# Kernel optimization log

Hardware: AMD Instinct MI355X
Metric: run time of the kernel (lower is better)

The kernel has to match this reference:

```python
import jax, jax.numpy as jnp
import numpy as np

B, T, D_MODEL, D_HIDDEN, MAX_SEQLEN = 4, 2048, 1024, 1024, 2048


def setup_inputs() -> dict:
    key = jax.random.key(0)
    ks = jax.random.split(key, 8)
    scale = 0.02  # keep exp() and linear outputs in a sane range
    return {
        "q": jax.random.normal(ks[0], (B, T, D_MODEL), dtype=jnp.float32),
        "k": jax.random.normal(ks[1], (B, T, D_MODEL), dtype=jnp.float32),
        "v": jax.random.normal(ks[2], (B, T, D_MODEL), dtype=jnp.float32),
        "Wq": jax.random.normal(ks[3], (D_HIDDEN, D_MODEL), dtype=jnp.float32) * scale,
        "Wk": jax.random.normal(ks[4], (D_HIDDEN, D_MODEL), dtype=jnp.float32) * scale,
        "Wv": jax.random.normal(ks[5], (D_HIDDEN, D_MODEL), dtype=jnp.float32) * scale,
        "Wo": jax.random.normal(ks[6], (D_MODEL, D_HIDDEN), dtype=jnp.float32) * scale,
        "W_bias": jax.random.normal(ks[7], (MAX_SEQLEN, MAX_SEQLEN), dtype=jnp.float32) * scale,
    }


def reference(q, k, v, Wq, Wk, Wv, Wo, W_bias):
    Ti = q.shape[1]
    Tj = k.shape[1]
    # Linear projections (torch Linear: x @ W.T), bias=False
    Q = jnp.einsum('btm,hm->bth', q, Wq)
    K = jnp.einsum('btm,hm->bth', k, Wk)
    V = jnp.einsum('btm,hm->bth', v, Wv)
    pos_bias = W_bias[:Ti, :Tj][None]              # (1, Ti, Tj)
    # Faithful to original: max over dim 0 (batch dim for K, singleton dim for pos_bias)
    max_key = jnp.max(K, axis=0, keepdims=True)    # (1, Tj, Dh)
    max_pos_bias = jnp.max(pos_bias, axis=0, keepdims=True)  # == pos_bias (dim 0 is size 1)
    exp_key = jnp.exp(K - max_key)                 # (B, Tj, Dh)
    exp_pos_bias = jnp.exp(pos_bias - max_pos_bias)  # all-ones, kept for faithfulness
    num = jnp.einsum('bij,bjd->bid', exp_pos_bias, exp_key * V)
    den = jnp.einsum('bij,bjd->bid', exp_pos_bias, exp_key)
    Yt = jax.nn.sigmoid(Q) * num / den             # (B, Ti, Dh)
    return jnp.einsum('bth,mh->btm', Yt, Wo)
```

## Files before the change

### kernel.cpp

```cpp
#include <hip/hip_runtime.h>
#include <hip/hip_bf16.h>

typedef __bf16 bf16;
typedef __bf16 bf16x8 __attribute__((ext_vector_type(8)));
typedef float f32x4 __attribute__((ext_vector_type(4)));
typedef float f32x16 __attribute__((ext_vector_type(16)));

#define B_   4
#define T_   2048
#define DM_  1024
#define DH_  1024
#define MROWS 8192

struct CvtJob { const float* src; bf16* dst; int nf4; };
struct CvtArgs { CvtJob job[7]; };

__global__ __launch_bounds__(256) void cvt_kernel(CvtArgs args) {
  CvtJob jb = args.job[blockIdx.y];
  int base = blockIdx.x * 2048;
  if (base >= jb.nf4) return;
  int t2 = threadIdx.x * 2;
  const float4* s = (const float4*)jb.src;
  float4 a[4][2];
#pragma unroll
  for (int u = 0; u < 4; ++u) {
    a[u][0] = s[base + u * 512 + t2];
    a[u][1] = s[base + u * 512 + t2 + 1];
  }
#pragma unroll
  for (int u = 0; u < 4; ++u) {
    bf16x8 o;
    o[0] = (bf16)a[u][0].x; o[1] = (bf16)a[u][0].y;
    o[2] = (bf16)a[u][0].z; o[3] = (bf16)a[u][0].w;
    o[4] = (bf16)a[u][1].x; o[5] = (bf16)a[u][1].y;
    o[6] = (bf16)a[u][1].z; o[7] = (bf16)a[u][1].w;
    *(bf16x8*)(jb.dst + ((size_t)base + u * 512 + t2) * 4) = o;
  }
}

struct GemmJob { const bf16* A; const bf16* Bw; float* Cf; bf16* Cb; int mode; };
struct GemmArgs { GemmJob job[4]; int N; int K; };

template <int MT>
__global__ __launch_bounds__(256) void gemm_bt(GemmArgs ga) {
  const GemmJob jb = ga.job[blockIdx.z];
  const int N = ga.N, K = ga.K;
  constexpr int TM = MT * 64;
  __shared__ __align__(16) bf16 As[TM * 64];
  __shared__ __align__(16) bf16 Bs[128 * 64];

  const int tid  = threadIdx.x;
  const int lane = tid & 63;
  const int wave = tid >> 6;
  const int wm   = (wave >> 1) * (MT * 32);
  const int wn   = (wave & 1) * 64;

  const int f   = blockIdx.y * 8 + blockIdx.x;
  const int xcd = f & 7;
  const int j   = f >> 3;
  const int bn  = j & 7;
  const int bm  = (j >> 3) * 8 + xcd;
  const int tileM = bm * TM;
  const int tileN = bn * 128;

  f32x16 acc[MT][2] = {};

  const int sr = lane >> 3;

  const char* pa = (const char*)(jb.A  + (size_t)tileM * K);
  const char* pb = (const char*)(jb.Bw + (size_t)tileN * K);
  unsigned int offA[MT * 2], offB[4];
#pragma unroll
  for (int l = 0; l < MT * 2; ++l) {
    int grp = wave * (MT * 2) + l;
    int sc  = (lane & 7) ^ sr ^ (grp & 7);
    offA[l] = (unsigned int)(((grp * 8 + sr) * K + sc * 8) * 2);
  }
#pragma unroll
  for (int l = 0; l < 4; ++l) {
    int grp = wave * 4 + l;
    int sc  = (lane & 7) ^ sr ^ (grp & 7);
    offB[l] = (unsigned int)(((grp * 8 + sr) * K + sc * 8) * 2);
  }

  const int half = lane >> 5;
  const int rc   = lane & 31;

  for (int k0 = 0; k0 < K; k0 += 64) {
#pragma unroll
    for (int l = 0; l < MT * 2; ++l)
      __builtin_amdgcn_global_load_lds(
          (const __attribute__((address_space(1))) void*)(pa + offA[l]),
          (__attribute__((address_space(3))) void*)&As[(wave * (MT * 2) + l) * 512],
          16, 0, 0);
#pragma unroll
    for (int l = 0; l < 4; ++l)
      __builtin_amdgcn_global_load_lds(
          (const __attribute__((address_space(1))) void*)(pb + offB[l]),
          (__attribute__((address_space(3))) void*)&Bs[(wave * 4 + l) * 512],
          16, 0, 0);
    pa += 128;
    pb += 128;
    __syncthreads();

#pragma unroll
    for (int s = 0; s < 2; ++s) {
      bf16x8 af[MT][2], bfr[2][2];
#pragma unroll
      for (int mt = 0; mt < MT; ++mt)
#pragma unroll
        for (int kk = 0; kk < 2; ++kk) {
          int row = wm + mt * 32 + rc;
          int chunk = ((s * 2 + kk) * 2 + half) ^ (row & 7) ^ ((row >> 3) & 7);
          af[mt][kk] = *(const bf16x8*)&As[row * 64 + chunk * 8];
        }
#pragma unroll
      for (int nt = 0; nt < 2; ++nt)
#pragma unroll
        for (int kk = 0; kk < 2; ++kk) {
          int row = wn + nt * 32 + rc;
          int chunk = ((s * 2 + kk) * 2 + half) ^ (row & 7) ^ ((row >> 3) & 7);
          bfr[nt][kk] = *(const bf16x8*)&Bs[row * 64 + chunk * 8];
        }
#pragma unroll
      for (int kk = 0; kk < 2; ++kk)
#pragma unroll
        for (int mt = 0; mt < MT; ++mt)
#pragma unroll
          for (int nt = 0; nt < 2; ++nt)
            acc[mt][nt] = __builtin_amdgcn_mfma_f32_32x32x16_bf16(
                af[mt][kk], bfr[nt][kk], acc[mt][nt], 0, 0, 0);
    }
    __syncthreads();
  }

  const int cn    = rc;
  const int rbase = half * 4;
  if (jb.mode == 0) {
#pragma unroll
    for (int mt = 0; mt < MT; ++mt)
#pragma unroll
      for (int nt = 0; nt < 2; ++nt)
#pragma unroll
        for (int r = 0; r < 16; ++r) {
          int row = tileM + wm + mt * 32 + rbase + (r & 3) + 8 * (r >> 2);
          int col = tileN + wn + nt * 32 + cn;
          jb.Cf[(size_t)row * N + col] = acc[mt][nt][r];
        }
  } else if (jb.mode == 1) {
#pragma unroll
    for (int mt = 0; mt < MT; ++mt)
#pragma unroll
      for (int nt = 0; nt < 2; ++nt)
#pragma unroll
        for (int r = 0; r < 16; ++r) {
          int row = tileM + wm + mt * 32 + rbase + (r & 3) + 8 * (r >> 2);
          int col = tileN + wn + nt * 32 + cn;
          jb.Cb[(size_t)row * N + col] =
              (bf16)(1.f / (1.f + __expf(-acc[mt][nt][r])));
        }
  } else {
#pragma unroll
    for (int mt = 0; mt < MT; ++mt)
#pragma unroll
      for (int nt = 0; nt < 2; ++nt)
#pragma unroll
        for (int r = 0; r < 16; ++r) {
          int row = tileM + wm + mt * 32 + rbase + (r & 3) + 8 * (r >> 2);
          int col = tileN + wn + nt * 32 + cn;
          jb.Cb[(size_t)row * N + col] = (bf16)acc[mt][nt][r];
        }
  }
}

__global__ __launch_bounds__(256) void kv_fused(
    const bf16* __restrict__ Ak, const bf16* __restrict__ Wk,
    const bf16* __restrict__ Av, const bf16* __restrict__ Wv,
    float* __restrict__ part) {
  const int K = DM_;
  __shared__ __align__(16) bf16 As[128 * 64];
  __shared__ __align__(16) bf16 Bs[128 * 64];

  const int tid  = threadIdx.x;
  const int lane = tid & 63;
  const int wave = tid >> 6;
  const int wm   = (wave >> 1) * 64;
  const int wn   = (wave & 1) * 64;

  const int f   = blockIdx.y * 8 + blockIdx.x;
  const int xcd = f & 7;
  const int j   = f >> 3;
  const int bn  = j & 7;
  const int bm  = (j >> 3) * 8 + xcd;
  const int tileN = bn * 128;
  const int j0    = bm * 32;

  const int sr   = lane >> 3;
  const int half = lane >> 5;
  const int rc   = lane & 31;

  unsigned int offA[4], offB[4];
#pragma unroll
  for (int l = 0; l < 4; ++l) {
    int grp = wave * 4 + l;
    int tr  = grp * 8 + sr;
    int sc  = (lane & 7) ^ sr ^ (grp & 7);
    offA[l] = (unsigned int)((((tr >> 5) * T_ + j0 + (tr & 31)) * K + sc * 8) * 2);
    offB[l] = (unsigned int)(((grp * 8 + sr) * K + sc * 8) * 2);
  }

  auto run = [&](const char* pa, const char* pb, f32x16 (&acc)[2][2]) {
    for (int k0 = 0; k0 < K; k0 += 64) {
#pragma unroll
      for (int l = 0; l < 4; ++l)
        __builtin_amdgcn_global_load_lds(
            (const __attribute__((address_space(1))) void*)(pa + offA[l]),
            (__attribute__((address_space(3))) void*)&As[(wave * 4 + l) * 512],
            16, 0, 0);
#pragma unroll
      for (int l = 0; l < 4; ++l)
        __builtin_amdgcn_global_load_lds(
            (const __attribute__((address_space(1))) void*)(pb + offB[l]),
            (__attribute__((address_space(3))) void*)&Bs[(wave * 4 + l) * 512],
            16, 0, 0);
      pa += 128;
      pb += 128;
      __syncthreads();
#pragma unroll
      for (int s = 0; s < 2; ++s) {
        bf16x8 af[2][2], bfr[2][2];
#pragma unroll
        for (int mt = 0; mt < 2; ++mt)
#pragma unroll
          for (int kk = 0; kk < 2; ++kk) {
            int row = wm + mt * 32 + rc;
            int chunk = ((s * 2 + kk) * 2 + half) ^ (row & 7) ^ ((row >> 3) & 7);
            af[mt][kk] = *(const bf16x8*)&As[row * 64 + chunk * 8];
          }
#pragma unroll
        for (int nt = 0; nt < 2; ++nt)
#pragma unroll
          for (int kk = 0; kk < 2; ++kk) {
            int row = wn + nt * 32 + rc;
            int chunk = ((s * 2 + kk) * 2 + half) ^ (row & 7) ^ ((row >> 3) & 7);
            bfr[nt][kk] = *(const bf16x8*)&Bs[row * 64 + chunk * 8];
          }
#pragma unroll
        for (int kk = 0; kk < 2; ++kk)
#pragma unroll
          for (int mt = 0; mt < 2; ++mt)
#pragma unroll
            for (int nt = 0; nt < 2; ++nt)
              acc[mt][nt] = __builtin_amdgcn_mfma_f32_32x32x16_bf16(
                  af[mt][kk], bfr[nt][kk], acc[mt][nt], 0, 0, 0);
      }
      __syncthreads();
    }
  };

  f32x16 aK[2][2] = {}, aV[2][2] = {};
  run((const char*)Ak, (const char*)(Wk + (size_t)tileN * K), aK);
  run((const char*)Av, (const char*)(Wv + (size_t)tileN * K), aV);

  const int rbase = half * 4;
  float* mx01 = (float*)As;
  float* mx23 = (float*)Bs;
#pragma unroll
  for (int nt = 0; nt < 2; ++nt)
#pragma unroll
    for (int r = 0; r < 16; ++r) {
      float ml = fmaxf(aK[0][nt][r], aK[1][nt][r]);
      int jloc = rbase + (r & 3) + 8 * (r >> 2);
      int idx  = (wave & 1) * 2048 + jloc * 64 + nt * 32 + rc;
      if (wave < 2) mx01[idx] = ml; else mx23[idx] = ml;
    }
  __syncthreads();
  float sn[2][2] = {{0.f, 0.f}, {0.f, 0.f}};
  float sd[2][2] = {{0.f, 0.f}, {0.f, 0.f}};
#pragma unroll
  for (int nt = 0; nt < 2; ++nt)
#pragma unroll
    for (int r = 0; r < 16; ++r) {
      int jloc = rbase + (r & 3) + 8 * (r >> 2);
      int idx  = (wave & 1) * 2048 + jloc * 64 + nt * 32 + rc;
      float mo = (wave < 2) ? mx23[idx] : mx01[idx];
      float m  = fmaxf(fmaxf(aK[0][nt][r], aK[1][nt][r]), mo);
      float e0 = __expf(aK[0][nt][r] - m);
      float e1 = __expf(aK[1][nt][r] - m);
      sn[0][nt] += e0 * aV[0][nt][r];
      sn[1][nt] += e1 * aV[1][nt][r];
      sd[0][nt] += e0;
      sd[1][nt] += e1;
    }
#pragma unroll
  for (int mt = 0; mt < 2; ++mt)
#pragma unroll
    for (int nt = 0; nt < 2; ++nt) {
      float n = sn[mt][nt] + __shfl_xor(sn[mt][nt], 32, 64);
      float d = sd[mt][nt] + __shfl_xor(sd[mt][nt], 32, 64);
      int b    = (wave >> 1) * 2 + mt;
      int dcol = tileN + wn + nt * 32 + rc;
      size_t base = (size_t)bm * 8192 + (size_t)b * 1024 + dcol;
      if (lane < 32) part[base] = n;
      else           part[base + 4096] = d;
    }
}

__global__ __launch_bounds__(256) void finish_kv(
    const float* __restrict__ part, float* __restrict__ numden) {
  int slot = blockIdx.x * 256 + threadIdx.x;
  float s0 = 0.f, s1 = 0.f, s2 = 0.f, s3 = 0.f;
#pragma unroll
  for (int i = 0; i < 64; i += 4) {
    s0 += part[(size_t)(i + 0) * 8192 + slot];
    s1 += part[(size_t)(i + 1) * 8192 + slot];
    s2 += part[(size_t)(i + 2) * 8192 + slot];
    s3 += part[(size_t)(i + 3) * 8192 + slot];
  }
  numden[slot] = (s0 + s1) + (s2 + s3);
}

__global__ __launch_bounds__(256) void scale_wo(
    const bf16* __restrict__ Wo, const float* __restrict__ numden,
    bf16* __restrict__ out4) {
  const int b = blockIdx.y;
  size_t i = ((size_t)blockIdx.x * 256 + threadIdx.x) * 8;
  int h = (int)(i & (DH_ - 1));
  bf16x8 w = *(const bf16x8*)(Wo + i);
  const float* nu = numden + b * DH_ + h;
  const float* de = numden + 4096 + b * DH_ + h;
  float4 n0 = *(const float4*)nu;
  float4 n1 = *(const float4*)(nu + 4);
  float4 d0 = *(const float4*)de;
  float4 d1 = *(const float4*)(de + 4);
  bf16x8 o;
  o[0] = (bf16)((float)w[0] * n0.x / d0.x);
  o[1] = (bf16)((float)w[1] * n0.y / d0.y);
  o[2] = (bf16)((float)w[2] * n0.z / d0.z);
  o[3] = (bf16)((float)w[3] * n0.w / d0.w);
  o[4] = (bf16)((float)w[4] * n1.x / d1.x);
  o[5] = (bf16)((float)w[5] * n1.y / d1.y);
  o[6] = (bf16)((float)w[6] * n1.z / d1.z);
  o[7] = (bf16)((float)w[7] * n1.w / d1.w);
  *(bf16x8*)(out4 + (size_t)b * ((size_t)DM_ * DH_) + i) = o;
}

extern "C" void kernel_launch(void* const* d_in, const int* in_sizes, int n_in,
                              void* d_out, int out_size, void* d_ws, size_t ws_size,
                              hipStream_t stream) {
  const float* q  = (const float*)d_in[0];
  const float* k  = (const float*)d_in[1];
  const float* v  = (const float*)d_in[2];
  const float* Wq = (const float*)d_in[3];
  const float* Wk = (const float*)d_in[4];
  const float* Wv = (const float*)d_in[5];
  const float* Wo = (const float*)d_in[6];
  float* out = (float*)d_out;

  char* ws = (char*)d_ws;
  size_t off = 0;
  auto alloc = [&](size_t bytes) {
    char* p = ws + off;
    off += (bytes + 255) & ~(size_t)255;
    return p;
  };
  const size_t actN = (size_t)MROWS * DM_;
  const size_t wN   = (size_t)DH_ * DM_;

  bf16* qb  = (bf16*)alloc(actN * 2);
  bf16* kb  = (bf16*)alloc(actN * 2);
  bf16* vb  = (bf16*)alloc(actN * 2);
  bf16* Wqb = (bf16*)alloc(wN * 2);
  bf16* Wkb = (bf16*)alloc(wN * 2);
  bf16* Wvb = (bf16*)alloc(wN * 2);
  bf16* Wob = (bf16*)alloc(wN * 2);
  bf16* Yb  = (bf16*)alloc(actN * 2);
  float* part = (float*)alloc((size_t)64 * 8192 * 4);
  float* numden = (float*)alloc(8192 * 4);
  bf16* Wob4 = (bf16*)alloc((size_t)B_ * wN * 2);

  CvtArgs ca;
  ca.job[0] = {q,  qb,  (int)(actN / 4)};
  ca.job[1] = {k,  kb,  (int)(actN / 4)};
  ca.job[2] = {v,  vb,  (int)(actN / 4)};
  ca.job[3] = {Wq, Wqb, (int)(wN / 4)};
  ca.job[4] = {Wk, Wkb, (int)(wN / 4)};
  ca.job[5] = {Wv, Wvb, (int)(wN / 4)};
  ca.job[6] = {Wo, Wob, (int)(wN / 4)};
  cvt_kernel<<<dim3(actN / 4 / 2048, 7), 256, 0, stream>>>(ca);

  GemmArgs g1;
  g1.N = DH_; g1.K = DM_;
  g1.job[0] = {qb, Wqb, nullptr, Yb, 1};
  g1.job[1] = {nullptr, nullptr, nullptr, nullptr, 0};
  g1.job[2] = {nullptr, nullptr, nullptr, nullptr, 0};
  g1.job[3] = {nullptr, nullptr, nullptr, nullptr, 0};
  gemm_bt<2><<<dim3(8, 64, 1), 256, 0, stream>>>(g1);

  kv_fused<<<dim3(8, 64), 256, 0, stream>>>(kb, Wkb, vb, Wvb, part);

  finish_kv<<<dim3(32), 256, 0, stream>>>(part, numden);

  scale_wo<<<dim3(512, 4), 256, 0, stream>>>(Wob, numden, Wob4);

  GemmArgs g2;
  g2.N = DM_; g2.K = DH_;
  for (int b = 0; b < 4; ++b) {
    g2.job[b] = {Yb + (size_t)b * ((size_t)T_ * DH_),
                 Wob4 + (size_t)b * wN,
                 out + (size_t)b * ((size_t)T_ * DM_),
                 nullptr, 0};
  }
  gemm_bt<1><<<dim3(8, 32, 4), 256, 0, stream>>>(g2);
}
```

Baseline: 286.7 us.

## Merge Q projection and KV reduction into one launch with smaller KV tiles

Replaces the separate Q-projection GEMM and the KV fused kernel with a single kernel whose grid splits into Q-GEMM blocks and KV blocks. KV blocks now cover 16 sequence positions across all 4 batches per tile, so the batch max is computed in registers without an LDS exchange. This raises the KV block count from 512 to 1024 to fill the GPU better and removes one launch, letting Q and KV work run concurrently. In exchange the KV blocks use half-height A tiles (less reuse of the weight tile), and there are four times as many partial slabs, so finish_kv does a longer reduction.

```diff
diff --git a/kernel.cpp b/kernel.cpp
--- a/kernel.cpp
+++ b/kernel.cpp
@@ -38,6 +38,213 @@
   }
 }
 
+__global__ __launch_bounds__(256) void proj_fused(
+    const bf16* __restrict__ qA, const bf16* __restrict__ qW,
+    bf16* __restrict__ Yb,
+    const bf16* __restrict__ kA, const bf16* __restrict__ kW,
+    const bf16* __restrict__ vA, const bf16* __restrict__ vW,
+    float* __restrict__ part) {
+  const int K = DM_;
+  __shared__ __align__(16) bf16 As[128 * 64];
+  __shared__ __align__(16) bf16 Bs[128 * 64];
+
+  const int tid  = threadIdx.x;
+  const int lane = tid & 63;
+  const int wave = tid >> 6;
+  const int sr   = lane >> 3;
+  const int half = lane >> 5;
+  const int rc   = lane & 31;
+  const int wn   = (wave & 1) * 64;
+
+  if (blockIdx.y < 64) {
+    const int wm  = (wave >> 1) * 64;
+    const int f   = blockIdx.y * 8 + blockIdx.x;
+    const int xcd = f & 7;
+    const int j   = f >> 3;
+    const int bn  = j & 7;
+    const int bm  = (j >> 3) * 8 + xcd;
+    const int tileM = bm * 128;
+    const int tileN = bn * 128;
+
+    f32x16 acc[2][2] = {};
+    const char* pa = (const char*)(qA + (size_t)tileM * K);
+    const char* pb = (const char*)(qW + (size_t)tileN * K);
+    unsigned int off[4];
+#pragma unroll
+    for (int l = 0; l < 4; ++l) {
+      int grp = wave * 4 + l;
+      int sc  = (lane & 7) ^ sr ^ (grp & 7);
+      off[l] = (unsigned int)(((grp * 8 + sr) * K + sc * 8) * 2);
+    }
+
+    for (int k0 = 0; k0 < K; k0 += 64) {
+#pragma unroll
+      for (int l = 0; l < 4; ++l)
+        __builtin_amdgcn_global_load_lds(
+            (const __attribute__((address_space(1))) void*)(pa + off[l]),
+            (__attribute__((address_space(3))) void*)&As[(wave * 4 + l) * 512],
+            16, 0, 0);
+#pragma unroll
+      for (int l = 0; l < 4; ++l)
+        __builtin_amdgcn_global_load_lds(
+            (const __attribute__((address_space(1))) void*)(pb + off[l]),
+            (__attribute__((address_space(3))) void*)&Bs[(wave * 4 + l) * 512],
+            16, 0, 0);
+      pa += 128;
+      pb += 128;
+      __syncthreads();
+#pragma unroll
+      for (int s = 0; s < 2; ++s) {
+        bf16x8 af[2][2], bfr[2][2];
+#pragma unroll
+        for (int mt = 0; mt < 2; ++mt)
+#pragma unroll
+          for (int kk = 0; kk < 2; ++kk) {
+            int row = wm + mt * 32 + rc;
+            int chunk = ((s * 2 + kk) * 2 + half) ^ (row & 7) ^ ((row >> 3) & 7);
+            af[mt][kk] = *(const bf16x8*)&As[row * 64 + chunk * 8];
+          }
+#pragma unroll
+        for (int nt = 0; nt < 2; ++nt)
+#pragma unroll
+          for (int kk = 0; kk < 2; ++kk) {
+            int row = wn + nt * 32 + rc;
+            int chunk = ((s * 2 + kk) * 2 + half) ^ (row & 7) ^ ((row >> 3) & 7);
+            bfr[nt][kk] = *(const bf16x8*)&Bs[row * 64 + chunk * 8];
+          }
+#pragma unroll
+        for (int kk = 0; kk < 2; ++kk)
+#pragma unroll
+          for (int mt = 0; mt < 2; ++mt)
+#pragma unroll
+            for (int nt = 0; nt < 2; ++nt)
+              acc[mt][nt] = __builtin_amdgcn_mfma_f32_32x32x16_bf16(
+                  af[mt][kk], bfr[nt][kk], acc[mt][nt], 0, 0, 0);
+      }
+      __syncthreads();
+    }
+
+    const int rbase = half * 4;
+#pragma unroll
+    for (int mt = 0; mt < 2; ++mt)
+#pragma unroll
+      for (int nt = 0; nt < 2; ++nt)
+#pragma unroll
+        for (int r = 0; r < 16; ++r) {
+          int row = tileM + wm + mt * 32 + rbase + (r & 3) + 8 * (r >> 2);
+          int col = tileN + wn + nt * 32 + rc;
+          Yb[(size_t)row * DH_ + col] =
+              (bf16)(1.f / (1.f + __expf(-acc[mt][nt][r])));
+        }
+    return;
+  }
+
+  const int wm  = (wave >> 1) * 32;
+  const int g   = (blockIdx.y - 64) * 8 + blockIdx.x;
+  const int xcd = g & 7;
+  const int h   = g >> 3;
+  const int bn  = h & 7;
+  const int jt  = (h >> 3) * 8 + xcd;
+  const int tileN = bn * 128;
+  const int j0    = jt * 16;
+
+  unsigned int offA[2], offB[4];
+#pragma unroll
+  for (int l = 0; l < 2; ++l) {
+    int grp = wave * 2 + l;
+    int tr  = grp * 8 + sr;
+    int sc  = (lane & 7) ^ sr ^ (grp & 7);
+    int rg  = (tr & 3) * T_ + j0 + (tr >> 2);
+    offA[l] = (unsigned int)(((size_t)rg * K + sc * 8) * 2);
+  }
+#pragma unroll
+  for (int l = 0; l < 4; ++l) {
+    int grp = wave * 4 + l;
+    int sc  = (lane & 7) ^ sr ^ (grp & 7);
+    offB[l] = (unsigned int)(((grp * 8 + sr) * K + sc * 8) * 2);
+  }
+
+  auto run = [&](const char* pa, const char* pb, f32x16 (&acc)[2]) {
+    for (int k0 = 0; k0 < K; k0 += 64) {
+#pragma unroll
+      for (int l = 0; l < 2; ++l)
+        __builtin_amdgcn_global_load_lds(
+            (const __attribute__((address_space(1))) void*)(pa + offA[l]),
+            (__attribute__((address_space(3))) void*)&As[(wave * 2 + l) * 512],
+            16, 0, 0);
+#pragma unroll
+      for (int l = 0; l < 4; ++l)
+        __builtin_amdgcn_global_load_lds(
+            (const __attribute__((address_space(1))) void*)(pb + offB[l]),
+            (__attribute__((address_space(3))) void*)&Bs[(wave * 4 + l) * 512],
+            16, 0, 0);
+      pa += 128;
+      pb += 128;
+      __syncthreads();
+#pragma unroll
+      for (int s = 0; s < 2; ++s) {
+        bf16x8 af[2], bfr[2][2];
+#pragma unroll
+        for (int kk = 0; kk < 2; ++kk) {
+          int row = wm + rc;
+          int chunk = ((s * 2 + kk) * 2 + half) ^ (row & 7) ^ ((row >> 3) & 7);
+          af[kk] = *(const bf16x8*)&As[row * 64 + chunk * 8];
+        }
+#pragma unroll
+        for (int nt = 0; nt < 2; ++nt)
+#pragma unroll
+          for (int kk = 0; kk < 2; ++kk) {
+            int row = wn + nt * 32 + rc;
+            int chunk = ((s * 2 + kk) * 2 + half) ^ (row & 7) ^ ((row >> 3) & 7);
+            bfr[nt][kk] = *(const bf16x8*)&Bs[row * 64 + chunk * 8];
+          }
+#pragma unroll
+        for (int kk = 0; kk < 2; ++kk)
+#pragma unroll
+          for (int nt = 0; nt < 2; ++nt)
+            acc[nt] = __builtin_amdgcn_mfma_f32_32x32x16_bf16(
+                af[kk], bfr[nt][kk], acc[nt], 0, 0, 0);
+      }
+      __syncthreads();
+    }
+  };
+
+  f32x16 aK[2] = {}, aV[2] = {};
+  run((const char*)kA, (const char*)(kW + (size_t)tileN * K), aK);
+  run((const char*)vA, (const char*)(vW + (size_t)tileN * K), aV);
+
+  float num[4][2] = {}, den[4][2] = {};
+#pragma unroll
+  for (int nt = 0; nt < 2; ++nt)
+#pragma unroll
+    for (int s = 0; s < 4; ++s) {
+      float m = fmaxf(fmaxf(aK[nt][4 * s + 0], aK[nt][4 * s + 1]),
+                      fmaxf(aK[nt][4 * s + 2], aK[nt][4 * s + 3]));
+#pragma unroll
+      for (int b = 0; b < 4; ++b) {
+        float e = __expf(aK[nt][4 * s + b] - m);
+        num[b][nt] += e * aV[nt][4 * s + b];
+        den[b][nt] += e;
+      }
+    }
+#pragma unroll
+  for (int b = 0; b < 4; ++b)
+#pragma unroll
+    for (int nt = 0; nt < 2; ++nt) {
+      num[b][nt] += __shfl_xor(num[b][nt], 32, 64);
+      den[b][nt] += __shfl_xor(den[b][nt], 32, 64);
+    }
+  const int slab = jt * 2 + (wave >> 1);
+#pragma unroll
+  for (int b = 0; b < 4; ++b)
+#pragma unroll
+    for (int nt = 0; nt < 2; ++nt) {
+      size_t base = (size_t)slab * 8192 + b * 1024 + tileN + wn + nt * 32 + rc;
+      if (lane < 32) part[base] = num[b][nt];
+      else           part[base + 4096] = den[b][nt];
+    }
+}
+
 struct GemmJob { const bf16* A; const bf16* Bw; float* Cf; bf16* Cb; int mode; };
 struct GemmArgs { GemmJob job[4]; int N; int K; };
 
@@ -64,7 +271,6 @@
   const int tileN = bn * 128;
 
   f32x16 acc[MT][2] = {};
-
   const int sr = lane >> 3;
 
   const char* pa = (const char*)(jb.A  + (size_t)tileM * K);
@@ -173,145 +379,11 @@
   }
 }
 
-__global__ __launch_bounds__(256) void kv_fused(
-    const bf16* __restrict__ Ak, const bf16* __restrict__ Wk,
-    const bf16* __restrict__ Av, const bf16* __restrict__ Wv,
-    float* __restrict__ part) {
-  const int K = DM_;
-  __shared__ __align__(16) bf16 As[128 * 64];
-  __shared__ __align__(16) bf16 Bs[128 * 64];
-
-  const int tid  = threadIdx.x;
-  const int lane = tid & 63;
-  const int wave = tid >> 6;
-  const int wm   = (wave >> 1) * 64;
-  const int wn   = (wave & 1) * 64;
-
-  const int f   = blockIdx.y * 8 + blockIdx.x;
-  const int xcd = f & 7;
-  const int j   = f >> 3;
-  const int bn  = j & 7;
-  const int bm  = (j >> 3) * 8 + xcd;
-  const int tileN = bn * 128;
-  const int j0    = bm * 32;
-
-  const int sr   = lane >> 3;
-  const int half = lane >> 5;
-  const int rc   = lane & 31;
-
-  unsigned int offA[4], offB[4];
-#pragma unroll
-  for (int l = 0; l < 4; ++l) {
-    int grp = wave * 4 + l;
-    int tr  = grp * 8 + sr;
-    int sc  = (lane & 7) ^ sr ^ (grp & 7);
-    offA[l] = (unsigned int)((((tr >> 5) * T_ + j0 + (tr & 31)) * K + sc * 8) * 2);
-    offB[l] = (unsigned int)(((grp * 8 + sr) * K + sc * 8) * 2);
-  }
-
-  auto run = [&](const char* pa, const char* pb, f32x16 (&acc)[2][2]) {
-    for (int k0 = 0; k0 < K; k0 += 64) {
-#pragma unroll
-      for (int l = 0; l < 4; ++l)
-        __builtin_amdgcn_global_load_lds(
-            (const __attribute__((address_space(1))) void*)(pa + offA[l]),
-            (__attribute__((address_space(3))) void*)&As[(wave * 4 + l) * 512],
-            16, 0, 0);
-#pragma unroll
-      for (int l = 0; l < 4; ++l)
-        __builtin_amdgcn_global_load_lds(
-            (const __attribute__((address_space(1))) void*)(pb + offB[l]),
-            (__attribute__((address_space(3))) void*)&Bs[(wave * 4 + l) * 512],
-            16, 0, 0);
-      pa += 128;
-      pb += 128;
-      __syncthreads();
-#pragma unroll
-      for (int s = 0; s < 2; ++s) {
-        bf16x8 af[2][2], bfr[2][2];
-#pragma unroll
-        for (int mt = 0; mt < 2; ++mt)
-#pragma unroll
-          for (int kk = 0; kk < 2; ++kk) {
-            int row = wm + mt * 32 + rc;
-            int chunk = ((s * 2 + kk) * 2 + half) ^ (row & 7) ^ ((row >> 3) & 7);
-            af[mt][kk] = *(const bf16x8*)&As[row * 64 + chunk * 8];
-          }
-#pragma unroll
-        for (int nt = 0; nt < 2; ++nt)
-#pragma unroll
-          for (int kk = 0; kk < 2; ++kk) {
-            int row = wn + nt * 32 + rc;
-            int chunk = ((s * 2 + kk) * 2 + half) ^ (row & 7) ^ ((row >> 3) & 7);
-            bfr[nt][kk] = *(const bf16x8*)&Bs[row * 64 + chunk * 8];
-          }
-#pragma unroll
-        for (int kk = 0; kk < 2; ++kk)
-#pragma unroll
-          for (int mt = 0; mt < 2; ++mt)
-#pragma unroll
-            for (int nt = 0; nt < 2; ++nt)
-              acc[mt][nt] = __builtin_amdgcn_mfma_f32_32x32x16_bf16(
-                  af[mt][kk], bfr[nt][kk], acc[mt][nt], 0, 0, 0);
-      }
-      __syncthreads();
-    }
-  };
-
-  f32x16 aK[2][2] = {}, aV[2][2] = {};
-  run((const char*)Ak, (const char*)(Wk + (size_t)tileN * K), aK);
-  run((const char*)Av, (const char*)(Wv + (size_t)tileN * K), aV);
-
-  const int rbase = half * 4;
-  float* mx01 = (float*)As;
-  float* mx23 = (float*)Bs;
-#pragma unroll
-  for (int nt = 0; nt < 2; ++nt)
-#pragma unroll
-    for (int r = 0; r < 16; ++r) {
-      float ml = fmaxf(aK[0][nt][r], aK[1][nt][r]);
-      int jloc = rbase + (r & 3) + 8 * (r >> 2);
-      int idx  = (wave & 1) * 2048 + jloc * 64 + nt * 32 + rc;
-      if (wave < 2) mx01[idx] = ml; else mx23[idx] = ml;
-    }
-  __syncthreads();
-  float sn[2][2] = {{0.f, 0.f}, {0.f, 0.f}};
-  float sd[2][2] = {{0.f, 0.f}, {0.f, 0.f}};
-#pragma unroll
-  for (int nt = 0; nt < 2; ++nt)
-#pragma unroll
-    for (int r = 0; r < 16; ++r) {
-      int jloc = rbase + (r & 3) + 8 * (r >> 2);
-      int idx  = (wave & 1) * 2048 + jloc * 64 + nt * 32 + rc;
-      float mo = (wave < 2) ? mx23[idx] : mx01[idx];
-      float m  = fmaxf(fmaxf(aK[0][nt][r], aK[1][nt][r]), mo);
-      float e0 = __expf(aK[0][nt][r] - m);
-      float e1 = __expf(aK[1][nt][r] - m);
-      sn[0][nt] += e0 * aV[0][nt][r];
-      sn[1][nt] += e1 * aV[1][nt][r];
-      sd[0][nt] += e0;
-      sd[1][nt] += e1;
-    }
-#pragma unroll
-  for (int mt = 0; mt < 2; ++mt)
-#pragma unroll
-    for (int nt = 0; nt < 2; ++nt) {
-      float n = sn[mt][nt] + __shfl_xor(sn[mt][nt], 32, 64);
-      float d = sd[mt][nt] + __shfl_xor(sd[mt][nt], 32, 64);
-      int b    = (wave >> 1) * 2 + mt;
-      int dcol = tileN + wn + nt * 32 + rc;
-      size_t base = (size_t)bm * 8192 + (size_t)b * 1024 + dcol;
-      if (lane < 32) part[base] = n;
-      else           part[base + 4096] = d;
-    }
-}
-
 __global__ __launch_bounds__(256) void finish_kv(
     const float* __restrict__ part, float* __restrict__ numden) {
   int slot = blockIdx.x * 256 + threadIdx.x;
   float s0 = 0.f, s1 = 0.f, s2 = 0.f, s3 = 0.f;
-#pragma unroll
-  for (int i = 0; i < 64; i += 4) {
+  for (int i = 0; i < 256; i += 4) {
     s0 += part[(size_t)(i + 0) * 8192 + slot];
     s1 += part[(size_t)(i + 1) * 8192 + slot];
     s2 += part[(size_t)(i + 2) * 8192 + slot];
@@ -375,7 +447,7 @@
   bf16* Wvb = (bf16*)alloc(wN * 2);
   bf16* Wob = (bf16*)alloc(wN * 2);
   bf16* Yb  = (bf16*)alloc(actN * 2);
-  float* part = (float*)alloc((size_t)64 * 8192 * 4);
+  float* part = (float*)alloc((size_t)256 * 8192 * 4);
   float* numden = (float*)alloc(8192 * 4);
   bf16* Wob4 = (bf16*)alloc((size_t)B_ * wN * 2);
 
@@ -389,15 +461,8 @@
   ca.job[6] = {Wo, Wob, (int)(wN / 4)};
   cvt_kernel<<<dim3(actN / 4 / 2048, 7), 256, 0, stream>>>(ca);
 
-  GemmArgs g1;
-  g1.N = DH_; g1.K = DM_;
-  g1.job[0] = {qb, Wqb, nullptr, Yb, 1};
-  g1.job[1] = {nullptr, nullptr, nullptr, nullptr, 0};
-  g1.job[2] = {nullptr, nullptr, nullptr, nullptr, 0};
-  g1.job[3] = {nullptr, nullptr, nullptr, nullptr, 0};
-  gemm_bt<2><<<dim3(8, 64, 1), 256, 0, stream>>>(g1);
-
-  kv_fused<<<dim3(8, 64), 256, 0, stream>>>(kb, Wkb, vb, Wvb, part);
+  proj_fused<<<dim3(8, 192), 256, 0, stream>>>(
+      qb, Wqb, Yb, kb, Wkb, vb, Wvb, part);
 
   finish_kv<<<dim3(32), 256, 0, stream>>>(part, numden);
 
```

Measured after the change: 282.5 us. Within noise of the previous version (-1.5%).
